# Performance work log

Hardware: AMD Instinct MI355X
Metric: run time of the kernel (lower is better)

## Reference

```python
import jax, jax.numpy as jnp
import numpy as np

D_MODEL, N_HEADS, D_K, D_V = 512, 8, 32, 32
LN_EPS = 1e-5


def setup_inputs() -> dict:
    key = jax.random.key(0)
    ks = jax.random.split(key, 12)
    B, L = 4, 2048
    inner = N_HEADS * D_K
    s_in = 1.0 / np.sqrt(D_MODEL)
    s_fc = 1.0 / np.sqrt(inner)
    return {
        "q": jax.random.normal(ks[0], (B, L, D_MODEL), jnp.float32),
        "k": jax.random.normal(ks[1], (B, L, D_MODEL), jnp.float32),
        "v": jax.random.normal(ks[2], (B, L, D_MODEL), jnp.float32),
        "Wq": jax.random.normal(ks[3], (inner, D_MODEL), jnp.float32) * s_in,
        "bq": jax.random.normal(ks[4], (inner,), jnp.float32) * 0.01,
        "Wk": jax.random.normal(ks[5], (inner, D_MODEL), jnp.float32) * s_in,
        "bk": jax.random.normal(ks[6], (inner,), jnp.float32) * 0.01,
        "Wv": jax.random.normal(ks[7], (N_HEADS * D_V, D_MODEL), jnp.float32) * s_in,
        "bv": jax.random.normal(ks[8], (N_HEADS * D_V,), jnp.float32) * 0.01,
        "Wfc": jax.random.normal(ks[9], (D_MODEL, N_HEADS * D_V), jnp.float32) * s_fc,
        "bfc": jax.random.normal(ks[10], (D_MODEL,), jnp.float32) * 0.01,
        "gamma": jnp.ones((D_MODEL,), jnp.float32),
        "beta": jnp.zeros((D_MODEL,), jnp.float32),
    }


def reference(q, k, v, Wq, bq, Wk, bk, Wv, bv, Wfc, bfc, gamma, beta):
    n, l, _ = q.shape
    # Projection output interpreted as (..., d_k, n_heads): head idx is fastest dim
    def split_heads(x, W, b, dh):
        p = x @ W.T + b                     # [n, l, dh*H]
        return p.reshape(n, x.shape[1], dh, N_HEADS).transpose(0, 3, 1, 2)  # [n,H,l,dh]

    qh = split_heads(q, Wq, bq, D_K)
    kh = split_heads(k, Wk, bk, D_K)
    vh = split_heads(v, Wv, bv, D_V)

    scale = 1.0 / jnp.sqrt(jnp.asarray(D_K, q.dtype))
    scores = jnp.einsum('nhqd,nhkd->nhqk', qh, kh) * scale  # [n,H,L,L]
    att = jax.nn.softmax(scores, axis=-1)
    out = jnp.einsum('nhqk,nhkd->nhqd', att, vh)             # [n,H,L,d_v]
    out = out.transpose(0, 2, 1, 3).reshape(n, l, N_HEADS * D_V)

    fc = out @ Wfc.T + bfc
    x = fc + q  # residual
    mean = jnp.mean(x, axis=-1, keepdims=True)
    var = jnp.mean(jnp.square(x - mean), axis=-1, keepdims=True)
    return gamma * (x - mean) / jnp.sqrt(var + LN_EPS) + beta
```

## Files before the change

### kernel.cpp

```cpp
#include <hip/hip_runtime.h>
#include <math.h>

constexpr int Bn = 4, Ln = 2048, DM = 512, NH = 8, DKv = 32, INNER = 256;
constexpr int TTOK = Bn * Ln;
constexpr size_t HEAD_ELEMS = (size_t)Bn * NH * Ln * DKv;


typedef short short8 __attribute__((ext_vector_type(8)));
typedef short short4v __attribute__((ext_vector_type(4)));
typedef float floatx4 __attribute__((ext_vector_type(4)));
typedef float floatx16 __attribute__((ext_vector_type(16)));

constexpr size_t WB_OFF  = 12536832;
constexpr size_t WFCB_OFF = WB_OFF + 3 * 131072;

constexpr float C1 = 0.25505654f;

__device__ inline short f2bf(float x) {
  unsigned u = __builtin_bit_cast(unsigned, x);
  unsigned r = (u + 0x7FFFu + ((u >> 16) & 1u)) >> 16;
  return (short)r;
}

__global__ __launch_bounds__(256) void cvtw_kernel(
    const float* __restrict__ Wq, const float* __restrict__ Wk,
    const float* __restrict__ Wv, const float* __restrict__ Wfc,
    short* __restrict__ Wb, short* __restrict__ Wfcb)
{
  const int z = blockIdx.y;
  const float* src = z == 0 ? Wq : (z == 1 ? Wk : (z == 2 ? Wv : Wfc));
  short* dst = z < 3 ? Wb + (size_t)z * 131072 : Wfcb;
  const int idx = (blockIdx.x * 256 + threadIdx.x) * 4;
  float4 x = *(const float4*)&src[idx];
  *(short4v*)&dst[idx] = (short4v){f2bf(x.x), f2bf(x.y), f2bf(x.z), f2bf(x.w)};
}

__global__ __launch_bounds__(256) void proj_kernel(
    const float* __restrict__ q, const float* __restrict__ k, const float* __restrict__ v,
    const short* __restrict__ Wb,
    const float* __restrict__ bq, const float* __restrict__ bk,
    const float* __restrict__ bv,
    short* __restrict__ ws)
{
  const int mat = blockIdx.z;
  const float* X    = mat == 0 ? q  : (mat == 1 ? k  : v);
  const short* W    = Wb + (size_t)mat * 131072;
  const float* bias = mat == 0 ? bq : (mat == 1 ? bk : bv);
  short* outp = ws + (size_t)mat * HEAD_ELEMS;

  const int t0 = blockIdx.x * 64;
  const int hp = blockIdx.y;
  const int tid = threadIdx.x;
  const int col = tid & 15;
  const int quad = (tid & 63) >> 4;
  const int w = tid >> 6;

  __shared__ short Xs[64 * 136];
  __shared__ short Wsh[64 * 136];

  floatx4 acc[4];
#pragma unroll
  for (int nj = 0; nj < 4; ++nj) acc[nj] = (floatx4){0.f, 0.f, 0.f, 0.f};

  float4 xr[8];
  short8 wr[4];
  auto loadX = [&](int k0) {
#pragma unroll
    for (int j = 0; j < 8; ++j) {
      const int i = tid + j * 256, row = i >> 5, c4 = i & 31;
      xr[j] = *(const float4*)&X[(size_t)(t0 + row) * DM + k0 + c4 * 4];
    }
  };
  auto loadW = [&](int k0) {
#pragma unroll
    for (int j = 0; j < 4; ++j) {
      const int s = tid + j * 256, row = s >> 4, k8 = s & 15;
      const int wrow = ((row & 31) << 3) + 2 * hp + (row >> 5);
      wr[j] = *(const short8*)&W[(size_t)wrow * DM + k0 + k8 * 8];
    }
  };

  loadX(0);
  loadW(0);

  for (int kc = 0; kc < 4; ++kc) {
#pragma unroll
    for (int j = 0; j < 8; ++j) {
      const int i = tid + j * 256, row = i >> 5, c4 = i & 31;
      *(short4v*)&Xs[row * 136 + c4 * 4] =
          (short4v){f2bf(xr[j].x), f2bf(xr[j].y), f2bf(xr[j].z), f2bf(xr[j].w)};
    }
#pragma unroll
    for (int j = 0; j < 4; ++j) {
      const int s = tid + j * 256, row = s >> 4, k8 = s & 15;
      *(short8*)&Wsh[row * 136 + k8 * 8] = wr[j];
    }
    __syncthreads();
    if (kc < 3) {
      loadX((kc + 1) * 128);
      loadW((kc + 1) * 128);
    }
#pragma unroll
    for (int ks = 0; ks < 4; ++ks) {
      short8 a = *(const short8*)&Xs[(w * 16 + col) * 136 + ks * 32 + quad * 8];
#pragma unroll
      for (int nj = 0; nj < 4; ++nj) {
        short8 b = *(const short8*)&Wsh[(nj * 16 + col) * 136 + ks * 32 + quad * 8];
        acc[nj] = __builtin_amdgcn_mfma_f32_16x16x32_bf16(a, b, acc[nj], 0, 0, 0);
      }
    }
    __syncthreads();
  }

  short* Ct = Xs;
  const int n = t0 >> 11, llb = t0 & (Ln - 1);

  if (mat < 2) {
#pragma unroll
    for (int nj = 0; nj < 4; ++nj) {
      const int j = nj * 16 + col;
      const int c = ((j & 31) << 3) + 2 * hp + (j >> 5);
      const float bi = bias[c];
#pragma unroll
      for (int r = 0; r < 4; ++r) {
        float pv = acc[nj][r] + bi;
        if (mat == 0) pv *= C1;
        Ct[(w * 16 + quad * 4 + r) * 72 + j] = f2bf(pv);
      }
    }
    __syncthreads();
#pragma unroll
    for (int it = 0; it < 2; ++it) {
      const int cid = tid + it * 256;
      const int h_loc = cid >> 8, tok = (cid >> 2) & 63, o = cid & 3;
      short8 val = *(const short8*)&Ct[tok * 72 + h_loc * 32 + o * 8];
      const int h = 2 * hp + h_loc;
      *(short8*)&outp[((size_t)(n * NH + h) * Ln + llb + tok) * DKv + o * 8] = val;
    }
  } else {
#pragma unroll
    for (int nj = 0; nj < 4; ++nj) {
      const int j = nj * 16 + col;
      const int c = ((j & 31) << 3) + 2 * hp + (j >> 5);
      const float bi = bias[c];
      short4v pk = (short4v){f2bf(acc[nj][0] + bi), f2bf(acc[nj][1] + bi),
                             f2bf(acc[nj][2] + bi), f2bf(acc[nj][3] + bi)};
      *(short4v*)&Ct[j * 72 + w * 16 + quad * 4] = pk;
    }
    __syncthreads();
#pragma unroll
    for (int it = 0; it < 2; ++it) {
      const int cid = tid + it * 256;
      const int h_loc = cid >> 8, d = (cid >> 3) & 31, to = cid & 7;
      short8 val = *(const short8*)&Ct[(h_loc * 32 + d) * 72 + to * 8];
      const int h = 2 * hp + h_loc;
      *(short8*)&outp[((size_t)(n * NH + h) * DKv + d) * Ln + llb + to * 8] = val;
    }
  }
}

__global__ __launch_bounds__(256) void attn_kernel(const short* __restrict__ ws,
                                                   short* __restrict__ O2b)
{
  const int bh = blockIdx.y;
  const int n = bh >> 3, h = bh & 7;
  const int tid = threadIdx.x;
  const int lane = tid & 63;
  const int col = lane & 31;
  const int hf = lane >> 5;
  const int w = tid >> 6;
  const int qi = blockIdx.x * 128 + w * 32 + col;

  const short* Qh = ws;
  const short* Kg = ws + HEAD_ELEMS + (size_t)bh * Ln * DKv;
  const short* Vg = ws + 2 * HEAD_ELEMS + (size_t)bh * DKv * Ln;

  __shared__ short Ks[2][128 * 40];
  __shared__ short Vs[2][32 * 136];

  short8 aq[2];
#pragma unroll
  for (int c = 0; c < 2; ++c)
    aq[c] = *(const short8*)&Qh[(size_t)bh * Ln * DKv + (size_t)qi * DKv + c * 16 + hf * 8];

  short8 ones;
#pragma unroll
  for (int j = 0; j < 8; ++j) ones[j] = (short)0x3F80;

  floatx16 o, ol;
#pragma unroll
  for (int i = 0; i < 16; ++i) { o[i] = 0.f; ol[i] = 0.f; }

  const int kg = tid >> 1, khalf = tid & 1;
  const int krow = (kg & ~12) | ((kg & 4) << 1) | ((kg & 8) >> 1);
  const int kst = krow * 40 + khalf * 16;
  const int vd = tid >> 3, vkb = tid & 7;
  const int vst = vd * 136 + vkb * 16;

  short8 kr0 = *(const short8*)(Kg + kg * 32 + khalf * 16);
  short8 kr1 = *(const short8*)(Kg + kg * 32 + khalf * 16 + 8);
  short8 vr0 = *(const short8*)(Vg + (size_t)vd * Ln + vkb * 16);
  short8 vr1 = *(const short8*)(Vg + (size_t)vd * Ln + vkb * 16 + 8);

  for (int kt = 0; kt < 16; ++kt) {
    short* ksb = Ks[kt & 1];
    short* vsb = Vs[kt & 1];
    *(short8*)&ksb[kst] = kr0;
    *(short8*)&ksb[kst + 8] = kr1;
    *(short8*)&vsb[vst] = vr0;
    *(short8*)&vsb[vst + 8] = vr1;
    __syncthreads();
    if (kt < 15) {
      kr0 = *(const short8*)(Kg + (size_t)(kt + 1) * 4096 + kg * 32 + khalf * 16);
      kr1 = *(const short8*)(Kg + (size_t)(kt + 1) * 4096 + kg * 32 + khalf * 16 + 8);
      vr0 = *(const short8*)(Vg + (size_t)vd * Ln + (kt + 1) * 128 + vkb * 16);
      vr1 = *(const short8*)(Vg + (size_t)vd * Ln + (kt + 1) * 128 + vkb * 16 + 8);
    }

#pragma unroll
    for (int cc = 0; cc < 4; ++cc) {
      floatx16 st;
#pragma unroll
      for (int i = 0; i < 16; ++i) st[i] = 0.f;
      short8 kf0 = *(const short8*)&ksb[(cc * 32 + col) * 40 + hf * 8];
      short8 kf1 = *(const short8*)&ksb[(cc * 32 + col) * 40 + 16 + hf * 8];
      st = __builtin_amdgcn_mfma_f32_32x32x16_bf16(kf0, aq[0], st, 0, 0, 0);
      st = __builtin_amdgcn_mfma_f32_32x32x16_bf16(kf1, aq[1], st, 0, 0, 0);

      float p[16];
#pragma unroll
      for (int i = 0; i < 16; ++i) p[i] = __builtin_amdgcn_exp2f(st[i]);
      short8 pf[2];
#pragma unroll
      for (int half = 0; half < 2; ++half) {
        unsigned u[4];
#pragma unroll
        for (int j = 0; j < 4; ++j)
          u[j] = __builtin_amdgcn_perm(
              __builtin_bit_cast(unsigned, p[half * 8 + 2 * j + 1]),
              __builtin_bit_cast(unsigned, p[half * 8 + 2 * j]), 0x07060302u);
        uint4 uu = make_uint4(u[0], u[1], u[2], u[3]);
        pf[half] = __builtin_bit_cast(short8, uu);
      }

      ol = __builtin_amdgcn_mfma_f32_32x32x16_bf16(ones, pf[0], ol, 0, 0, 0);
      ol = __builtin_amdgcn_mfma_f32_32x32x16_bf16(ones, pf[1], ol, 0, 0, 0);

      short8 va0 = *(const short8*)&vsb[col * 136 + cc * 32 + hf * 8];
      short8 va1 = *(const short8*)&vsb[col * 136 + cc * 32 + 16 + hf * 8];
      o = __builtin_amdgcn_mfma_f32_32x32x16_bf16(va0, pf[0], o, 0, 0, 0);
      o = __builtin_amdgcn_mfma_f32_32x32x16_bf16(va1, pf[1], o, 0, 0, 0);
    }
  }

  const float inv = 1.f / ol[0];
  short* dst = &O2b[((size_t)n * Ln + qi) * INNER + h * DKv];
#pragma unroll
  for (int g4 = 0; g4 < 4; ++g4) {
    short4v pk = (short4v){f2bf(o[g4 * 4 + 0] * inv), f2bf(o[g4 * 4 + 1] * inv),
                           f2bf(o[g4 * 4 + 2] * inv), f2bf(o[g4 * 4 + 3] * inv)};
    *(short4v*)&dst[8 * g4 + 4 * hf] = pk;
  }
}

__global__ __launch_bounds__(256) void fcln_kernel(
    const short* __restrict__ O2b, const short* __restrict__ Wfcb,
    const float* __restrict__ bfc, const float* __restrict__ qin,
    const float* __restrict__ gamma, const float* __restrict__ beta,
    float* __restrict__ outp)
{
  const int t0 = blockIdx.x * 16;
  const int tid = threadIdx.x;
  const int col = tid & 15;
  const int quad = (tid & 63) >> 4;
  const int w = tid >> 6;

  __shared__ short As[16 * 264];
  __shared__ float sred[2][16][4];

  {
    const int row = tid >> 4, k16 = tid & 15;
    *(short8*)&As[row * 264 + k16 * 16] =
        *(const short8*)&O2b[(size_t)(t0 + row) * INNER + k16 * 16];
    *(short8*)&As[row * 264 + k16 * 16 + 8] =
        *(const short8*)&O2b[(size_t)(t0 + row) * INNER + k16 * 16 + 8];
  }
  __syncthreads();

  const short* Wp = Wfcb + (size_t)(w * 128 + col) * INNER + quad * 8;

  floatx4 acc[8];
#pragma unroll
  for (int nj = 0; nj < 8; ++nj) acc[nj] = (floatx4){0.f, 0.f, 0.f, 0.f};

#pragma unroll
  for (int ks = 0; ks < 8; ++ks) {
    short8 a = *(const short8*)&As[col * 264 + ks * 32 + quad * 8];
#pragma unroll
    for (int nj = 0; nj < 8; ++nj) {
      short8 b = *(const short8*)&Wp[(size_t)nj * 16 * INNER + ks * 32];
      acc[nj] = __builtin_amdgcn_mfma_f32_16x16x32_bf16(a, b, acc[nj], 0, 0, 0);
    }
  }

  float s1[4], s2[4];
#pragma unroll
  for (int r = 0; r < 4; ++r) { s1[r] = 0.f; s2[r] = 0.f; }

#pragma unroll
  for (int nj = 0; nj < 8; ++nj) {
    const int c = w * 128 + nj * 16 + col;
    const float bi = bfc[c];
#pragma unroll
    for (int r = 0; r < 4; ++r) {
      const int t = t0 + quad * 4 + r;
      float x = acc[nj][r] + bi + qin[(size_t)t * DM + c];
      acc[nj][r] = x;
      s1[r] += x;
      s2[r] += x * x;
    }
  }
#pragma unroll
  for (int r = 0; r < 4; ++r) {
#pragma unroll
    for (int off = 1; off <= 8; off <<= 1) {
      s1[r] += __shfl_xor(s1[r], off);
      s2[r] += __shfl_xor(s2[r], off);
    }
  }
  if (col == 0) {
#pragma unroll
    for (int r = 0; r < 4; ++r) {
      sred[0][quad * 4 + r][w] = s1[r];
      sred[1][quad * 4 + r][w] = s2[r];
    }
  }
  __syncthreads();

  float mean[4], rstd[4];
#pragma unroll
  for (int r = 0; r < 4; ++r) {
    const int tk = quad * 4 + r;
    const float S1 = sred[0][tk][0] + sred[0][tk][1] + sred[0][tk][2] + sred[0][tk][3];
    const float S2 = sred[1][tk][0] + sred[1][tk][1] + sred[1][tk][2] + sred[1][tk][3];
    mean[r] = S1 * (1.f / 512.f);
    const float var = S2 * (1.f / 512.f) - mean[r] * mean[r];
    rstd[r] = rsqrtf(var + 1e-5f);
  }

#pragma unroll
  for (int nj = 0; nj < 8; ++nj) {
    const int c = w * 128 + nj * 16 + col;
    const float g = gamma[c], bb = beta[c];
#pragma unroll
    for (int r = 0; r < 4; ++r) {
      const int t = t0 + quad * 4 + r;
      outp[(size_t)t * DM + c] = g * (acc[nj][r] - mean[r]) * rstd[r] + bb;
    }
  }
}

extern "C" void kernel_launch(void* const* d_in, const int* in_sizes, int n_in,
                              void* d_out, int out_size, void* d_ws, size_t ws_size,
                              hipStream_t stream) {
  const float* q     = (const float*)d_in[0];
  const float* k     = (const float*)d_in[1];
  const float* v     = (const float*)d_in[2];
  const float* Wq    = (const float*)d_in[3];
  const float* bq    = (const float*)d_in[4];
  const float* Wk    = (const float*)d_in[5];
  const float* bk    = (const float*)d_in[6];
  const float* Wv    = (const float*)d_in[7];
  const float* bv    = (const float*)d_in[8];
  const float* Wfc   = (const float*)d_in[9];
  const float* bfc   = (const float*)d_in[10];
  const float* gamma = (const float*)d_in[11];
  const float* beta  = (const float*)d_in[12];

  short* wsS  = (short*)d_ws;
  short* O2b  = wsS + 3 * HEAD_ELEMS;
  short* Wb   = wsS + WB_OFF;
  short* Wfcb = wsS + WFCB_OFF;

  cvtw_kernel<<<dim3(128, 4), 256, 0, stream>>>(Wq, Wk, Wv, Wfc, Wb, Wfcb);

  dim3 gp(TTOK / 64, 4, 3);
  proj_kernel<<<gp, 256, 0, stream>>>(q, k, v, Wb, bq, bk, bv, wsS);

  dim3 gatt(Ln / 128, Bn * NH);
  attn_kernel<<<gatt, 256, 0, stream>>>(wsS, O2b);

  fcln_kernel<<<dim3(TTOK / 16), 256, 0, stream>>>(O2b, Wfcb, bfc, q, gamma, beta,
                                                   (float*)d_out);
}
```

Baseline: 175.2 us.

## Compute all heads per projection block and remap attention blocks across XCDs

The projection kernel now has each block compute all 256 output columns for its 64 tokens, rather than splitting them across 4 head-pair blocks. Each X tile is read and converted to bf16 once instead of four times, using a smaller K chunk (64) and 16 accumulators per thread. The attention kernel remaps its linear block id so that all q-blocks of a given batch-head land on the same XCD, which should improve L2 reuse of K/V. The costs are higher register pressure and fewer projection blocks (384), which may reduce occupancy and parallelism.

```diff
diff --git a/kernel.cpp b/kernel.cpp
--- a/kernel.cpp
+++ b/kernel.cpp
@@ -42,106 +42,107 @@
     const float* __restrict__ bv,
     short* __restrict__ ws)
 {
-  const int mat = blockIdx.z;
+  const int mat = blockIdx.y;
   const float* X    = mat == 0 ? q  : (mat == 1 ? k  : v);
   const short* W    = Wb + (size_t)mat * 131072;
   const float* bias = mat == 0 ? bq : (mat == 1 ? bk : bv);
   short* outp = ws + (size_t)mat * HEAD_ELEMS;
 
   const int t0 = blockIdx.x * 64;
-  const int hp = blockIdx.y;
   const int tid = threadIdx.x;
   const int col = tid & 15;
   const int quad = (tid & 63) >> 4;
   const int w = tid >> 6;
 
-  __shared__ short Xs[64 * 136];
-  __shared__ short Wsh[64 * 136];
-
-  floatx4 acc[4];
-#pragma unroll
-  for (int nj = 0; nj < 4; ++nj) acc[nj] = (floatx4){0.f, 0.f, 0.f, 0.f};
-
-  float4 xr[8];
-  short8 wr[4];
+  __shared__ short smem[23040];
+  short* Xs  = smem;
+  short* Wsh = smem + 64 * 72;
+
+  floatx16 accv;
+  floatx4 acc[16];
+#pragma unroll
+  for (int nj = 0; nj < 16; ++nj) acc[nj] = (floatx4){0.f, 0.f, 0.f, 0.f};
+  (void)accv;
+
+  float4 xr[4];
+  short8 wr[8];
   auto loadX = [&](int k0) {
 #pragma unroll
-    for (int j = 0; j < 8; ++j) {
-      const int i = tid + j * 256, row = i >> 5, c4 = i & 31;
+    for (int j = 0; j < 4; ++j) {
+      const int i = tid + j * 256, row = i >> 4, c4 = i & 15;
       xr[j] = *(const float4*)&X[(size_t)(t0 + row) * DM + k0 + c4 * 4];
     }
   };
   auto loadW = [&](int k0) {
 #pragma unroll
-    for (int j = 0; j < 4; ++j) {
-      const int s = tid + j * 256, row = s >> 4, k8 = s & 15;
-      const int wrow = ((row & 31) << 3) + 2 * hp + (row >> 5);
-      wr[j] = *(const short8*)&W[(size_t)wrow * DM + k0 + k8 * 8];
+    for (int j = 0; j < 8; ++j) {
+      const int s = tid + j * 256, jrow = s >> 3, c8 = s & 7;
+      const int wrow = ((jrow & 31) << 3) + (jrow >> 5);
+      wr[j] = *(const short8*)&W[(size_t)wrow * DM + k0 + c8 * 8];
     }
   };
 
   loadX(0);
   loadW(0);
 
-  for (int kc = 0; kc < 4; ++kc) {
+  for (int kc = 0; kc < 8; ++kc) {
+#pragma unroll
+    for (int j = 0; j < 4; ++j) {
+      const int i = tid + j * 256, row = i >> 4, c4 = i & 15;
+      *(short4v*)&Xs[row * 72 + c4 * 4] =
+          (short4v){f2bf(xr[j].x), f2bf(xr[j].y), f2bf(xr[j].z), f2bf(xr[j].w)};
+    }
 #pragma unroll
     for (int j = 0; j < 8; ++j) {
-      const int i = tid + j * 256, row = i >> 5, c4 = i & 31;
-      *(short4v*)&Xs[row * 136 + c4 * 4] =
-          (short4v){f2bf(xr[j].x), f2bf(xr[j].y), f2bf(xr[j].z), f2bf(xr[j].w)};
-    }
-#pragma unroll
-    for (int j = 0; j < 4; ++j) {
-      const int s = tid + j * 256, row = s >> 4, k8 = s & 15;
-      *(short8*)&Wsh[row * 136 + k8 * 8] = wr[j];
+      const int s = tid + j * 256, jrow = s >> 3, c8 = s & 7;
+      *(short8*)&Wsh[jrow * 72 + c8 * 8] = wr[j];
     }
     __syncthreads();
-    if (kc < 3) {
-      loadX((kc + 1) * 128);
-      loadW((kc + 1) * 128);
-    }
-#pragma unroll
-    for (int ks = 0; ks < 4; ++ks) {
-      short8 a = *(const short8*)&Xs[(w * 16 + col) * 136 + ks * 32 + quad * 8];
-#pragma unroll
-      for (int nj = 0; nj < 4; ++nj) {
-        short8 b = *(const short8*)&Wsh[(nj * 16 + col) * 136 + ks * 32 + quad * 8];
+    if (kc < 7) {
+      loadX((kc + 1) * 64);
+      loadW((kc + 1) * 64);
+    }
+#pragma unroll
+    for (int ks = 0; ks < 2; ++ks) {
+      short8 a = *(const short8*)&Xs[(w * 16 + col) * 72 + ks * 32 + quad * 8];
+#pragma unroll
+      for (int nj = 0; nj < 16; ++nj) {
+        short8 b = *(const short8*)&Wsh[(nj * 16 + col) * 72 + ks * 32 + quad * 8];
         acc[nj] = __builtin_amdgcn_mfma_f32_16x16x32_bf16(a, b, acc[nj], 0, 0, 0);
       }
     }
     __syncthreads();
   }
 
-  short* Ct = Xs;
+  short* Ct = smem;
   const int n = t0 >> 11, llb = t0 & (Ln - 1);
 
   if (mat < 2) {
 #pragma unroll
-    for (int nj = 0; nj < 4; ++nj) {
+    for (int nj = 0; nj < 16; ++nj) {
       const int j = nj * 16 + col;
-      const int c = ((j & 31) << 3) + 2 * hp + (j >> 5);
+      const int c = ((j & 31) << 3) + (j >> 5);
       const float bi = bias[c];
 #pragma unroll
       for (int r = 0; r < 4; ++r) {
         float pv = acc[nj][r] + bi;
         if (mat == 0) pv *= C1;
-        Ct[(w * 16 + quad * 4 + r) * 72 + j] = f2bf(pv);
+        Ct[(w * 16 + quad * 4 + r) * 268 + j] = f2bf(pv);
       }
     }
     __syncthreads();
 #pragma unroll
-    for (int it = 0; it < 2; ++it) {
+    for (int it = 0; it < 8; ++it) {
       const int cid = tid + it * 256;
-      const int h_loc = cid >> 8, tok = (cid >> 2) & 63, o = cid & 3;
-      short8 val = *(const short8*)&Ct[tok * 72 + h_loc * 32 + o * 8];
-      const int h = 2 * hp + h_loc;
+      const int h = cid >> 8, tok = (cid >> 2) & 63, o = cid & 3;
+      short8 val = *(const short8*)&Ct[tok * 268 + h * 32 + o * 8];
       *(short8*)&outp[((size_t)(n * NH + h) * Ln + llb + tok) * DKv + o * 8] = val;
     }
   } else {
 #pragma unroll
-    for (int nj = 0; nj < 4; ++nj) {
+    for (int nj = 0; nj < 16; ++nj) {
       const int j = nj * 16 + col;
-      const int c = ((j & 31) << 3) + 2 * hp + (j >> 5);
+      const int c = ((j & 31) << 3) + (j >> 5);
       const float bi = bias[c];
       short4v pk = (short4v){f2bf(acc[nj][0] + bi), f2bf(acc[nj][1] + bi),
                              f2bf(acc[nj][2] + bi), f2bf(acc[nj][3] + bi)};
@@ -149,11 +150,11 @@
     }
     __syncthreads();
 #pragma unroll
-    for (int it = 0; it < 2; ++it) {
+    for (int it = 0; it < 8; ++it) {
       const int cid = tid + it * 256;
-      const int h_loc = cid >> 8, d = (cid >> 3) & 31, to = cid & 7;
-      short8 val = *(const short8*)&Ct[(h_loc * 32 + d) * 72 + to * 8];
-      const int h = 2 * hp + h_loc;
+      const int j = cid >> 3, to = cid & 7;
+      const int h = j >> 5, d = j & 31;
+      short8 val = *(const short8*)&Ct[j * 72 + to * 8];
       *(short8*)&outp[((size_t)(n * NH + h) * DKv + d) * Ln + llb + to * 8] = val;
     }
   }
@@ -162,14 +163,18 @@
 __global__ __launch_bounds__(256) void attn_kernel(const short* __restrict__ ws,
                                                    short* __restrict__ O2b)
 {
-  const int bh = blockIdx.y;
+  const int vid = blockIdx.x + 16 * blockIdx.y;
+  const int xcd = vid & 7, jj = vid >> 3;
+  const int bh = xcd * 4 + (jj >> 4);
+  const int qblk = jj & 15;
+
   const int n = bh >> 3, h = bh & 7;
   const int tid = threadIdx.x;
   const int lane = tid & 63;
   const int col = lane & 31;
   const int hf = lane >> 5;
   const int w = tid >> 6;
-  const int qi = blockIdx.x * 128 + w * 32 + col;
+  const int qi = qblk * 128 + w * 32 + col;
 
   const short* Qh = ws;
   const short* Kg = ws + HEAD_ELEMS + (size_t)bh * Ln * DKv;
@@ -384,7 +389,7 @@
 
   cvtw_kernel<<<dim3(128, 4), 256, 0, stream>>>(Wq, Wk, Wv, Wfc, Wb, Wfcb);
 
-  dim3 gp(TTOK / 64, 4, 3);
+  dim3 gp(TTOK / 64, 3);
   proj_kernel<<<gp, 256, 0, stream>>>(q, k, v, Wb, bq, bk, bv, wsS);
 
   dim3 gatt(Ln / 128, Bn * NH);
```

New measurement: 174.5 us. No clear change (-0.3%).
